# Kernel tuning notes

Hardware: AMD Instinct MI355X
Metric: run time of the kernel (lower is better)

## Reference

```python
import jax, jax.numpy as jnp
import numpy as np


def setup_inputs() -> dict:
    key = jax.random.key(0)
    k1, k2, k3 = jax.random.split(key, 3)
    early = jax.random.normal(k1, (64, 1, 512, 512), dtype=jnp.float32)
    middle = jax.random.normal(k2, (64, 1, 256, 256), dtype=jnp.float32)
    deep = jax.random.normal(k3, (64, 1, 128, 128), dtype=jnp.float32)
    return {"early": early, "middle": middle, "deep": deep, "max_features": 500000}


def reference(early, middle, deep, max_features):
    # Concatenate all scores and find the threshold = (max_features)-th entry of
    # the descending sort, i.e. the (max_features+1)-th largest value.
    all_scores = jnp.concatenate([early.ravel(), middle.ravel(), deep.ravel()])
    n = all_scores.shape[0]
    if max_features >= n:
        thresh = jnp.asarray(0.0, dtype=all_scores.dtype)
    else:
        # top_k(k+1)[-1] == sort(descending)[k]; avoids a full sort.
        topk_vals, _ = jax.lax.top_k(all_scores, max_features + 1)
        thresh = topk_vals[-1]
    thresh = jax.lax.stop_gradient(thresh)
    early_out = jnp.where(early < thresh, jnp.zeros((), early.dtype), early)
    middle_out = jnp.where(middle < thresh, jnp.zeros((), middle.dtype), middle)
    deep_out = jnp.where(deep < thresh, jnp.zeros((), deep.dtype), deep)
    return (early_out, middle_out, deep_out)
```

## Files before the change

### kernel.cpp

```cpp
#include <hip/hip_runtime.h>

typedef float nfloat4 __attribute__((ext_vector_type(4)));

#define WS_CANDCNT 0
#define WS_B1      1
#define WS_HIST1   16
#define WS_HIST2   272
#define WS_HIST3   4368
#define WS_ZEND    8464
#define WS_CAND    8464

#define STASH 2048

__device__ __forceinline__ unsigned fkey(float f) {
  unsigned x = __float_as_uint(f);
  return x ^ ((x & 0x80000000u) ? 0xFFFFFFFFu : 0x80000000u);
}
__device__ __forceinline__ float unkey(unsigned u) {
  unsigned x = u ^ ((u & 0x80000000u) ? 0x80000000u : 0xFFFFFFFFu);
  return __uint_as_float(x);
}

__device__ __forceinline__ unsigned block_scan_incl(unsigned v, unsigned* sh4) {
  const int t = threadIdx.x;
  unsigned p = v;
#pragma unroll
  for (int off = 1; off < 64; off <<= 1) {
    unsigned y = __shfl_up(p, off);
    if ((t & 63) >= off) p += y;
  }
  if ((t & 63) == 63) sh4[t >> 6] = p;
  __syncthreads();
  unsigned wo = 0;
  for (int w = 0; w < (t >> 6); ++w) wo += sh4[w];
  __syncthreads();
  return p + wo;
}

__device__ __forceinline__ uint2 select_desc256(const unsigned* __restrict__ gh,
                                                unsigned k, unsigned* sh4, unsigned* sel2) {
  const int t = threadIdx.x;
  unsigned cnt = gh[255 - t];
  unsigned incl = block_scan_incl(cnt, sh4);
  unsigned excl = incl - cnt;
  if (excl < k && incl >= k) { sel2[0] = (unsigned)(255 - t); sel2[1] = k - excl; }
  __syncthreads();
  uint2 r; r.x = sel2[0]; r.y = sel2[1];
  __syncthreads();
  return r;
}

__device__ __forceinline__ uint2 select_desc4096(const unsigned* __restrict__ gh,
                                                 unsigned k, unsigned* sh4, unsigned* sel2) {
  const int t = threadIdx.x;
  unsigned loc[16]; unsigned s = 0;
  const int base = 4095 - t * 16;
#pragma unroll
  for (int j = 0; j < 16; ++j) { unsigned c = gh[base - j]; loc[j] = c; s += c; }
  unsigned incl = block_scan_incl(s, sh4);
  unsigned excl = incl - s;
  if (excl < k && incl >= k) {
    unsigned cum = excl; int j = 0;
    while (cum + loc[j] < k) { cum += loc[j]; ++j; }
    sel2[0] = (unsigned)(base - j); sel2[1] = k - cum;
  }
  __syncthreads();
  uint2 r; r.x = sel2[0]; r.y = sel2[1];
  __syncthreads();
  return r;
}

__global__ void zero_ws(unsigned* __restrict__ ws) {
  int i = blockIdx.x * blockDim.x + threadIdx.x;
  if (i < WS_ZEND) ws[i] = 0u;
}

__global__ void __launch_bounds__(1024) hist1_kernel(
    const float* __restrict__ e, const float* __restrict__ m,
    const float* __restrict__ d, int n0v, int n1v, int n2v,
    unsigned* __restrict__ ws) {
  __shared__ unsigned h[256 * 32];
  for (int i = threadIdx.x; i < 256 * 32; i += 1024) h[i] = 0u;
  __syncthreads();
  const unsigned sub = threadIdx.x & 31u;
  const int gid = blockIdx.x * 1024 + threadIdx.x;
  const int G = gridDim.x * 1024;

  auto acc1 = [&](float4 f) {
    atomicAdd(&h[((fkey(f.x) >> 24) << 5) | sub], 1u);
    atomicAdd(&h[((fkey(f.y) >> 24) << 5) | sub], 1u);
    atomicAdd(&h[((fkey(f.z) >> 24) << 5) | sub], 1u);
    atomicAdd(&h[((fkey(f.w) >> 24) << 5) | sub], 1u);
  };
  auto sweep = [&](const float* src, int nv) {
    const float4* a4 = (const float4*)src;
    int v = gid;
    for (; v + 3 * G < nv; v += 4 * G) {
      float4 f0 = a4[v];
      float4 f1 = a4[v + G];
      float4 f2 = a4[v + 2 * G];
      float4 f3 = a4[v + 3 * G];
      acc1(f0); acc1(f1); acc1(f2); acc1(f3);
    }
    for (; v < nv; v += G) acc1(a4[v]);
  };
  sweep(e, n0v);
  sweep(m, n1v);
  sweep(d, n2v);
  __syncthreads();
  const int t = threadIdx.x;
  if (t < 256) {
    unsigned s = 0;
#pragma unroll
    for (int j = 0; j < 32; ++j) s += h[(t << 5) + ((t + j) & 31)];
    if (s) atomicAdd(&ws[WS_HIST1 + t], s);
  }
}

__global__ void __launch_bounds__(256) sel1_kernel(
    const int* __restrict__ maxf, unsigned* __restrict__ ws, long long n) {
  __shared__ unsigned sh4[4];
  __shared__ unsigned sel2[2];
  long long kk = (long long)maxf[0] + 1;
  if (kk > n) {
    if (threadIdx.x == 0) ws[WS_B1] = 0x80u;
    return;
  }
  uint2 r = select_desc256(ws + WS_HIST1, (unsigned)kk, sh4, sel2);
  if (threadIdx.x == 0) ws[WS_B1] = r.x;
}

__global__ void __launch_bounds__(1024) scatter_kernel(
    const float* __restrict__ e, const float* __restrict__ m, const float* __restrict__ d,
    float* __restrict__ out, unsigned* __restrict__ ws, unsigned cap,
    int e_blks, int m_blks) {
  const int t = threadIdx.x;
  const int bid = blockIdx.x;

  __shared__ float    sh_v[STASH];
  __shared__ unsigned sh_i[STASH];
  __shared__ unsigned sh_cnt;
  __shared__ unsigned sh_base;

  if (t == 0) sh_cnt = 0u;
  const unsigned b1 = ws[WS_B1];
  __syncthreads();

  const float4* in4;
  if (bid < e_blks)               in4 = (const float4*)e + (long long)bid * 2048;
  else if (bid < e_blks + m_blks) in4 = (const float4*)m + (long long)(bid - e_blks) * 2048;
  else                            in4 = (const float4*)d + (long long)(bid - e_blks - m_blks) * 2048;
  const int out_base_v = bid * 2048;
  nfloat4* out4 = (nfloat4*)out + out_base_v;

  float* gcV = (float*)(ws + WS_CAND);
  unsigned* gcI = ws + WS_CAND + cap;

  auto emit1 = [&](float4 f, int v) {
    unsigned kx = fkey(f.x), ky = fkey(f.y), kz = fkey(f.z), kw = fkey(f.w);
    nfloat4 o;
    o.x = ((kx >> 24) >= b1) ? f.x : 0.0f;
    o.y = ((ky >> 24) >= b1) ? f.y : 0.0f;
    o.z = ((kz >> 24) >= b1) ? f.z : 0.0f;
    o.w = ((kw >> 24) >= b1) ? f.w : 0.0f;
    __builtin_nontemporal_store(o, &out4[v]);
    unsigned ks[4] = {kx, ky, kz, kw};
    float fs[4] = {f.x, f.y, f.z, f.w};
#pragma unroll
    for (int cc = 0; cc < 4; ++cc) {
      if ((ks[cc] >> 24) == b1) {
        unsigned idx = (unsigned)(out_base_v + v) * 4u + (unsigned)cc;
        unsigned pos = atomicAdd(&sh_cnt, 1u);
        if (pos < STASH) { sh_v[pos] = fs[cc]; sh_i[pos] = idx; }
        else {
          unsigned g = atomicAdd(&ws[WS_CANDCNT], 1u);
          gcV[g] = fs[cc]; gcI[g] = idx;
        }
      }
    }
  };

  const int v0 = t;
  const int v1 = 1024 + t;
  float4 f0 = in4[v0];
  float4 f1 = in4[v1];
  emit1(f0, v0);
  emit1(f1, v1);

  __syncthreads();
  if (t == 0) {
    unsigned tot = sh_cnt < STASH ? sh_cnt : STASH;
    sh_base = tot ? atomicAdd(&ws[WS_CANDCNT], tot) : 0u;
    sh_cnt = tot;
  }
  __syncthreads();
  const unsigned tot = sh_cnt;
  const unsigned base = sh_base;
  for (unsigned i = t; i < tot; i += 1024) {
    gcV[base + i] = sh_v[i];
    gcI[base + i] = sh_i[i];
  }
}

__global__ void __launch_bounds__(256) candhist2_kernel(
    unsigned* __restrict__ ws, unsigned cap) {
  const int t = threadIdx.x;
  __shared__ unsigned sh_hist[4096];
  for (int i = t; i < 4096; i += 256) sh_hist[i] = 0u;
  __syncthreads();
  unsigned cnt = ws[WS_CANDCNT]; if (cnt > cap) cnt = cap;
  const float* candV = (const float*)(ws + WS_CAND);
  const unsigned G = gridDim.x * 256;
  for (unsigned i = blockIdx.x * 256 + t; i < cnt; i += G) {
    unsigned u = fkey(candV[i]);
    atomicAdd(&sh_hist[(u >> 12) & 0xFFFu], 1u);
  }
  __syncthreads();
  for (int i = t; i < 4096; i += 256) {
    unsigned v = sh_hist[i];
    if (v) atomicAdd(&ws[WS_HIST2 + i], v);
  }
}

__global__ void __launch_bounds__(256) candhist3_kernel(
    const int* __restrict__ maxf, unsigned* __restrict__ ws, unsigned cap, long long n) {
  const int t = threadIdx.x;
  __shared__ unsigned sh_hist[4096];
  __shared__ unsigned sh4[4];
  __shared__ unsigned sel2[2];
  for (int i = t; i < 4096; i += 256) sh_hist[i] = 0u;

  long long kk = (long long)maxf[0] + 1;
  unsigned pfx;
  if (kk > n) {
    pfx = 0x80u << 12;
    __syncthreads();
  } else {
    uint2 r1 = select_desc256(ws + WS_HIST1, (unsigned)kk, sh4, sel2);
    uint2 r2 = select_desc4096(ws + WS_HIST2, r1.y, sh4, sel2);
    pfx = (r1.x << 12) | r2.x;
  }
  __syncthreads();

  unsigned cnt = ws[WS_CANDCNT]; if (cnt > cap) cnt = cap;
  const float* candV = (const float*)(ws + WS_CAND);
  const unsigned G = gridDim.x * 256;
  for (unsigned i = blockIdx.x * 256 + t; i < cnt; i += G) {
    unsigned u = fkey(candV[i]);
    if ((u >> 12) == pfx) atomicAdd(&sh_hist[u & 0xFFFu], 1u);
  }
  __syncthreads();
  for (int i = t; i < 4096; i += 256) {
    unsigned v = sh_hist[i];
    if (v) atomicAdd(&ws[WS_HIST3 + i], v);
  }
}

__global__ void __launch_bounds__(256) fixup_kernel(
    float* __restrict__ out, const int* __restrict__ maxf,
    unsigned* __restrict__ ws, unsigned cap, long long n) {
  const int t = threadIdx.x;
  __shared__ unsigned sh4[4];
  __shared__ unsigned sel2[2];

  long long kk = (long long)maxf[0] + 1;
  float th;
  if (kk > n) {
    th = 0.0f;
    __syncthreads();
  } else {
    uint2 r1 = select_desc256(ws + WS_HIST1, (unsigned)kk, sh4, sel2);
    uint2 r2 = select_desc4096(ws + WS_HIST2, r1.y, sh4, sel2);
    uint2 r3 = select_desc4096(ws + WS_HIST3, r2.y, sh4, sel2);
    th = unkey((r1.x << 24) | (r2.x << 12) | r3.x);
  }

  unsigned cnt = ws[WS_CANDCNT]; if (cnt > cap) cnt = cap;
  const float* candV = (const float*)(ws + WS_CAND);
  const unsigned* candI = ws + WS_CAND + cap;
  const unsigned G = gridDim.x * 256;
  for (unsigned i = blockIdx.x * 256 + t; i < cnt; i += G) {
    float f = candV[i];
    if (f < th) out[candI[i]] = 0.0f;
  }
}

extern "C" void kernel_launch(void* const* d_in, const int* in_sizes, int n_in,
                              void* d_out, int out_size, void* d_ws, size_t ws_size,
                              hipStream_t stream) {
  const float* e = (const float*)d_in[0];
  const float* m = (const float*)d_in[1];
  const float* d = (const float*)d_in[2];
  const int* maxf = (const int*)d_in[3];
  float* out = (float*)d_out;
  unsigned* ws = (unsigned*)d_ws;

  const long long n0 = in_sizes[0], n1 = in_sizes[1], n2 = in_sizes[2];
  const long long n = n0 + n1 + n2;
  const int n0v = (int)(n0 / 4), n1v = (int)(n1 / 4), n2v = (int)(n2 / 4);

  long long capll = ((long long)(ws_size / 4) - WS_CAND) / 2;
  if (capll < 0) capll = 0;
  if (capll > n) capll = n;
  const unsigned cap = (unsigned)capll;

  const int e_blks = (int)(n0 / 8192), m_blks = (int)(n1 / 8192);
  const int nblocks = (int)(n / 8192);

  zero_ws<<<(WS_ZEND + 255) / 256, 256, 0, stream>>>(ws);
  hist1_kernel<<<512, 1024, 0, stream>>>(e, m, d, n0v, n1v, n2v, ws);
  sel1_kernel<<<1, 256, 0, stream>>>(maxf, ws, n);
  scatter_kernel<<<nblocks, 1024, 0, stream>>>(e, m, d, out, ws, cap, e_blks, m_blks);
  candhist2_kernel<<<128, 256, 0, stream>>>(ws, cap);
  candhist3_kernel<<<128, 256, 0, stream>>>(maxf, ws, cap, n);
  fixup_kernel<<<256, 256, 0, stream>>>(out, maxf, ws, cap, n);
}
```

Measured before the change: 212.8 us.

## Fold second-level histogram into scatter and reuse stored radix-select results

Removes the separate candhist2 kernel. The second-level histogram is now built inside the scatter kernel with global atomics as candidates are flushed from shared memory. sel1 and candhist3 write their selected prefix and remaining rank to the workspace, so later kernels read them instead of redoing the earlier selection passes. Scatter blocks now process four float4 per thread instead of two, halving the block count. This saves a launch and a full reread of the candidate buffer, at the cost of many contended global atomics on the histogram bins.

```diff
diff --git a/kernel.cpp b/kernel.cpp
--- a/kernel.cpp
+++ b/kernel.cpp
@@ -4,6 +4,9 @@
 
 #define WS_CANDCNT 0
 #define WS_B1      1
+#define WS_K2      2
+#define WS_PFX     3
+#define WS_K3      4
 #define WS_HIST1   16
 #define WS_HIST2   272
 #define WS_HIST3   4368
@@ -127,7 +130,7 @@
     return;
   }
   uint2 r = select_desc256(ws + WS_HIST1, (unsigned)kk, sh4, sel2);
-  if (threadIdx.x == 0) ws[WS_B1] = r.x;
+  if (threadIdx.x == 0) { ws[WS_B1] = r.x; ws[WS_K2] = r.y; }
 }
 
 __global__ void __launch_bounds__(1024) scatter_kernel(
@@ -147,15 +150,27 @@
   __syncthreads();
 
   const float4* in4;
-  if (bid < e_blks)               in4 = (const float4*)e + (long long)bid * 2048;
-  else if (bid < e_blks + m_blks) in4 = (const float4*)m + (long long)(bid - e_blks) * 2048;
-  else                            in4 = (const float4*)d + (long long)(bid - e_blks - m_blks) * 2048;
-  const int out_base_v = bid * 2048;
+  if (bid < e_blks)               in4 = (const float4*)e + (long long)bid * 4096;
+  else if (bid < e_blks + m_blks) in4 = (const float4*)m + (long long)(bid - e_blks) * 4096;
+  else                            in4 = (const float4*)d + (long long)(bid - e_blks - m_blks) * 4096;
+  const int out_base_v = bid * 4096;
   nfloat4* out4 = (nfloat4*)out + out_base_v;
 
   float* gcV = (float*)(ws + WS_CAND);
   unsigned* gcI = ws + WS_CAND + cap;
 
+  auto push = [&](unsigned key, float v, int vidx, int cc) {
+    if ((key >> 24) == b1) {
+      unsigned idx = (unsigned)(out_base_v + vidx) * 4u + (unsigned)cc;
+      unsigned pos = atomicAdd(&sh_cnt, 1u);
+      if (pos < STASH) { sh_v[pos] = v; sh_i[pos] = idx; }
+      else {
+        unsigned g = atomicAdd(&ws[WS_CANDCNT], 1u);
+        gcV[g] = v; gcI[g] = idx;
+        atomicAdd(&ws[WS_HIST2 + ((key >> 12) & 0xFFFu)], 1u);
+      }
+    }
+  };
   auto emit1 = [&](float4 f, int v) {
     unsigned kx = fkey(f.x), ky = fkey(f.y), kz = fkey(f.z), kw = fkey(f.w);
     nfloat4 o;
@@ -164,28 +179,18 @@
     o.z = ((kz >> 24) >= b1) ? f.z : 0.0f;
     o.w = ((kw >> 24) >= b1) ? f.w : 0.0f;
     __builtin_nontemporal_store(o, &out4[v]);
-    unsigned ks[4] = {kx, ky, kz, kw};
-    float fs[4] = {f.x, f.y, f.z, f.w};
-#pragma unroll
-    for (int cc = 0; cc < 4; ++cc) {
-      if ((ks[cc] >> 24) == b1) {
-        unsigned idx = (unsigned)(out_base_v + v) * 4u + (unsigned)cc;
-        unsigned pos = atomicAdd(&sh_cnt, 1u);
-        if (pos < STASH) { sh_v[pos] = fs[cc]; sh_i[pos] = idx; }
-        else {
-          unsigned g = atomicAdd(&ws[WS_CANDCNT], 1u);
-          gcV[g] = fs[cc]; gcI[g] = idx;
-        }
-      }
-    }
+    push(kx, f.x, v, 0); push(ky, f.y, v, 1);
+    push(kz, f.z, v, 2); push(kw, f.w, v, 3);
   };
 
-  const int v0 = t;
-  const int v1 = 1024 + t;
-  float4 f0 = in4[v0];
-  float4 f1 = in4[v1];
-  emit1(f0, v0);
-  emit1(f1, v1);
+  float4 f0 = in4[t];
+  float4 f1 = in4[1024 + t];
+  float4 f2 = in4[2048 + t];
+  float4 f3 = in4[3072 + t];
+  emit1(f0, t);
+  emit1(f1, 1024 + t);
+  emit1(f2, 2048 + t);
+  emit1(f3, 3072 + t);
 
   __syncthreads();
   if (t == 0) {
@@ -197,28 +202,10 @@
   const unsigned tot = sh_cnt;
   const unsigned base = sh_base;
   for (unsigned i = t; i < tot; i += 1024) {
-    gcV[base + i] = sh_v[i];
+    float v = sh_v[i];
+    gcV[base + i] = v;
     gcI[base + i] = sh_i[i];
-  }
-}
-
-__global__ void __launch_bounds__(256) candhist2_kernel(
-    unsigned* __restrict__ ws, unsigned cap) {
-  const int t = threadIdx.x;
-  __shared__ unsigned sh_hist[4096];
-  for (int i = t; i < 4096; i += 256) sh_hist[i] = 0u;
-  __syncthreads();
-  unsigned cnt = ws[WS_CANDCNT]; if (cnt > cap) cnt = cap;
-  const float* candV = (const float*)(ws + WS_CAND);
-  const unsigned G = gridDim.x * 256;
-  for (unsigned i = blockIdx.x * 256 + t; i < cnt; i += G) {
-    unsigned u = fkey(candV[i]);
-    atomicAdd(&sh_hist[(u >> 12) & 0xFFFu], 1u);
-  }
-  __syncthreads();
-  for (int i = t; i < 4096; i += 256) {
-    unsigned v = sh_hist[i];
-    if (v) atomicAdd(&ws[WS_HIST2 + i], v);
+    atomicAdd(&ws[WS_HIST2 + ((fkey(v) >> 12) & 0xFFFu)], 1u);
   }
 }
 
@@ -236,9 +223,11 @@
     pfx = 0x80u << 12;
     __syncthreads();
   } else {
-    uint2 r1 = select_desc256(ws + WS_HIST1, (unsigned)kk, sh4, sel2);
-    uint2 r2 = select_desc4096(ws + WS_HIST2, r1.y, sh4, sel2);
-    pfx = (r1.x << 12) | r2.x;
+    unsigned b1 = ws[WS_B1];
+    unsigned k2 = ws[WS_K2];
+    uint2 r2 = select_desc4096(ws + WS_HIST2, k2, sh4, sel2);
+    pfx = (b1 << 12) | r2.x;
+    if (blockIdx.x == 0 && t == 0) { ws[WS_PFX] = pfx; ws[WS_K3] = r2.y; }
   }
   __syncthreads();
 
@@ -269,10 +258,10 @@
     th = 0.0f;
     __syncthreads();
   } else {
-    uint2 r1 = select_desc256(ws + WS_HIST1, (unsigned)kk, sh4, sel2);
-    uint2 r2 = select_desc4096(ws + WS_HIST2, r1.y, sh4, sel2);
-    uint2 r3 = select_desc4096(ws + WS_HIST3, r2.y, sh4, sel2);
-    th = unkey((r1.x << 24) | (r2.x << 12) | r3.x);
+    unsigned pfx = ws[WS_PFX];
+    unsigned k3  = ws[WS_K3];
+    uint2 r3 = select_desc4096(ws + WS_HIST3, k3, sh4, sel2);
+    th = unkey((pfx << 12) | r3.x);
   }
 
   unsigned cnt = ws[WS_CANDCNT]; if (cnt > cap) cnt = cap;
@@ -304,14 +293,13 @@
   if (capll > n) capll = n;
   const unsigned cap = (unsigned)capll;
 
-  const int e_blks = (int)(n0 / 8192), m_blks = (int)(n1 / 8192);
-  const int nblocks = (int)(n / 8192);
+  const int e_blks = (int)(n0 / 16384), m_blks = (int)(n1 / 16384);
+  const int nblocks = (int)(n / 16384);
 
   zero_ws<<<(WS_ZEND + 255) / 256, 256, 0, stream>>>(ws);
   hist1_kernel<<<512, 1024, 0, stream>>>(e, m, d, n0v, n1v, n2v, ws);
   sel1_kernel<<<1, 256, 0, stream>>>(maxf, ws, n);
   scatter_kernel<<<nblocks, 1024, 0, stream>>>(e, m, d, out, ws, cap, e_blks, m_blks);
-  candhist2_kernel<<<128, 256, 0, stream>>>(ws, cap);
   candhist3_kernel<<<128, 256, 0, stream>>>(maxf, ws, cap, n);
   fixup_kernel<<<256, 256, 0, stream>>>(out, maxf, ws, cap, n);
 }
```

Measured after the change: 327.4 us. 1.54x slower.
